# Performance work log

Measured on AMD Instinct MI355X. Metric: run time of the kernel, lower is better.

Reference implementation:

```python
import jax, jax.numpy as jnp
import numpy as np

ALPHA = 0.2  # LeakyReLU negative slope
MASK_FILL = -9e15


def setup_inputs() -> dict:
    key = jax.random.key(0)
    k1, k2, k3, k4 = jax.random.split(key, 4)
    N, F_IN, F_OUT = 8192, 128, 64
    x = jax.random.normal(k1, (N, F_IN), dtype=jnp.float32)
    adj = jax.random.randint(k2, (N, N), 0, 2, dtype=jnp.int32)
    # xavier_uniform with gain=1.414 (approx sqrt(2))
    gain = 1.414
    lim_w = gain * np.sqrt(6.0 / (F_IN + F_OUT))
    W = jax.random.uniform(k3, (F_IN, F_OUT), minval=-lim_w, maxval=lim_w, dtype=jnp.float32)
    lim_a = gain * np.sqrt(6.0 / (2 * F_OUT + 1))
    a = jax.random.uniform(k4, (2 * F_OUT, 1), minval=-lim_a, maxval=lim_a, dtype=jnp.float32)
    return {"x": x, "adj": adj, "W": W, "a": a}


def reference(x, adj, W, a):
    # h: [N, F_out]
    h = x @ W
    f_out = h.shape[1]
    # Decompose a^T [h_i || h_j] = h_i . a1 + h_j . a2 (exactly the same math,
    # avoids materializing the N*N*2F concat tensor).
    a1 = a[:f_out, 0]  # [F_out]
    a2 = a[f_out:, 0]  # [F_out]
    e = (h @ a1)[:, None] + (h @ a2)[None, :]  # [N, N]
    e = jax.nn.leaky_relu(e, negative_slope=ALPHA)
    e = jnp.where(adj > 0, e, MASK_FILL)
    attention = jax.nn.softmax(e, axis=1)  # row-wise softmax
    h_prime = attention @ h  # [N, F_out]
    return jax.nn.elu(h_prime)  # concat=True branch
```

## Files before the change

kernel.cpp:

```cpp
#include <hip/hip_runtime.h>
#include <math.h>

#define NN 8192
#define FIN 128
#define FOUT 64
#define LRELU 0.2f
#define JSPLIT 8
#define BI 64
#define PASTR 72
#define HTSTR 72

typedef _Float16 f16x8 __attribute__((ext_vector_type(8)));
typedef _Float16 f16x4 __attribute__((ext_vector_type(4)));
typedef float f32x4 __attribute__((ext_vector_type(4)));

#define WS_HT 0
#define WS_S1 262144
#define WS_S2 270336
#define WS_S2MAX 278528
#define WS_PACC 278544
#define WS_LP (WS_PACC + JSPLIT * NN * FOUT)

__global__ __launch_bounds__(256) void k_hs(const float* __restrict__ x,
                                            const float* __restrict__ W,
                                            const float* __restrict__ a,
                                            float* ws) {
  __shared__ float Wl[FIN * FOUT];
  __shared__ float xl[16 * FIN];
  __shared__ float hl[16 * FOUT];
  const int t = threadIdx.x;
  const int i0 = blockIdx.x * 16;

#pragma unroll
  for (int c = 0; c < 8; ++c) {
    const int flat = c * 1024 + t * 4;
    *(float4*)&Wl[flat] = *(const float4*)&W[flat];
  }
#pragma unroll
  for (int c = 0; c < 2; ++c) {
    const int flat = c * 1024 + t * 4;
    *(float4*)&xl[flat] = *(const float4*)&x[(size_t)i0 * FIN + flat];
  }
  __syncthreads();

  const int r = t >> 4;
  const int fg = t & 15;
  float4 acc = make_float4(0.f, 0.f, 0.f, 0.f);
#pragma unroll 4
  for (int k = 0; k < FIN; ++k) {
    const float xv = xl[r * FIN + k];
    const float4 wv = *(const float4*)&Wl[k * FOUT + fg * 4];
    acc.x = fmaf(xv, wv.x, acc.x);
    acc.y = fmaf(xv, wv.y, acc.y);
    acc.z = fmaf(xv, wv.z, acc.z);
    acc.w = fmaf(xv, wv.w, acc.w);
  }

  float v1 = acc.x * a[fg * 4] + acc.y * a[fg * 4 + 1] +
             acc.z * a[fg * 4 + 2] + acc.w * a[fg * 4 + 3];
  float v2 = acc.x * a[FOUT + fg * 4] + acc.y * a[FOUT + fg * 4 + 1] +
             acc.z * a[FOUT + fg * 4 + 2] + acc.w * a[FOUT + fg * 4 + 3];
  v1 += __shfl_xor(v1, 1); v2 += __shfl_xor(v2, 1);
  v1 += __shfl_xor(v1, 2); v2 += __shfl_xor(v2, 2);
  v1 += __shfl_xor(v1, 4); v2 += __shfl_xor(v2, 4);
  v1 += __shfl_xor(v1, 8); v2 += __shfl_xor(v2, 8);
  if (fg == 0) {
    ws[WS_S1 + i0 + r] = v1;
    ws[WS_S2 + i0 + r] = v2;
  }

  *(float4*)&hl[r * FOUT + fg * 4] = acc;
  __syncthreads();
  _Float16* ht = (_Float16*)(ws + WS_HT);
  if (t < 128) {
    const int f = t >> 1;
    const int off = (t & 1) * 8;
    f16x8 tmp;
#pragma unroll
    for (int u = 0; u < 8; ++u) tmp[u] = (_Float16)hl[(off + u) * FOUT + f];
    *(f16x8*)&ht[(size_t)f * NN + i0 + off] = tmp;
  }
}

__global__ __launch_bounds__(256) void k_s2max(float* ws) {
  __shared__ float red[256];
  const int t = threadIdx.x;
  float v = -1e30f;
#pragma unroll
  for (int i = 0; i < NN / 256; ++i) v = fmaxf(v, ws[WS_S2 + i * 256 + t]);
  red[t] = v;
  __syncthreads();
  for (int s = 128; s >= 1; s >>= 1) {
    if (t < s) red[t] = fmaxf(red[t], red[t + s]);
    __syncthreads();
  }
  if (t == 0) ws[WS_S2MAX] = red[0];
}

__global__ __launch_bounds__(256) void k_main(const int* __restrict__ adj,
                                              float* ws) {
  __shared__ __align__(16) _Float16 pal[BI * PASTR];
  __shared__ __align__(16) _Float16 htl[FOUT * HTSTR];
  __shared__ float s1l[BI], mll[BI];

  const int t = threadIdx.x;
  const int ib = blockIdx.x >> 3;
  const int js = blockIdx.x & 7;
  const int i0 = ib * BI;
  const int jbase = js * (NN / JSPLIT);

  const _Float16* ht = (const _Float16*)(ws + WS_HT);
  const float s2max = ws[WS_S2MAX];
  if (t < BI) {
    const float s1v = ws[WS_S1 + i0 + t];
    s1l[t] = s1v;
    const float tmp = s1v + s2max;
    mll[t] = fmaxf(tmp, LRELU * tmp);
  }

  f32x4 acc[4];
#pragma unroll
  for (int nf = 0; nf < 4; ++nf) acc[nf] = (f32x4){0.f, 0.f, 0.f, 0.f};
  float lacc[4] = {0.f, 0.f, 0.f, 0.f};

  const int jg = t & 15;
  const int ig = t >> 4;
  const int w = t >> 6;
  const int l = t & 63;

  __syncthreads();

  for (int tile = 0; tile < (NN / JSPLIT) / 64; ++tile) {
    const int j0 = jbase + tile * 64;

#pragma unroll
    for (int c2 = 0; c2 < 2; ++c2) {
      const int chunk = t + c2 * 256;
      const int n = chunk >> 3, off = (chunk & 7) * 8;
      *(f16x8*)&htl[n * HTSTR + off] = *(const f16x8*)&ht[(size_t)n * NN + j0 + off];
    }

    const float4 s2v = *(const float4*)&ws[WS_S2 + j0 + jg * 4];
#pragma unroll
    for (int c = 0; c < 4; ++c) {
      const int il = ig + c * 16;
      const int4 av = *(const int4*)&adj[(size_t)(i0 + il) * NN + j0 + jg * 4];
      const float s1v = s1l[il], mv = mll[il];
      float e0 = s1v + s2v.x; e0 = fmaxf(e0, LRELU * e0);
      float e1 = s1v + s2v.y; e1 = fmaxf(e1, LRELU * e1);
      float e2 = s1v + s2v.z; e2 = fmaxf(e2, LRELU * e2);
      float e3 = s1v + s2v.w; e3 = fmaxf(e3, LRELU * e3);
      const _Float16 p0 = av.x > 0 ? (_Float16)__expf(e0 - mv) : (_Float16)0.f;
      const _Float16 p1 = av.y > 0 ? (_Float16)__expf(e1 - mv) : (_Float16)0.f;
      const _Float16 p2 = av.z > 0 ? (_Float16)__expf(e2 - mv) : (_Float16)0.f;
      const _Float16 p3 = av.w > 0 ? (_Float16)__expf(e3 - mv) : (_Float16)0.f;
      lacc[c] += ((float)p0 + (float)p1) + ((float)p2 + (float)p3);
      f16x4 pv = {p0, p1, p2, p3};
      *(f16x4*)&pal[il * PASTR + jg * 4] = pv;
    }
    __syncthreads();

    {
      const int mrow = w * 16 + (l & 15);
      const int q8 = (l >> 4) * 8;
      const f16x8 a0 = *(const f16x8*)&pal[mrow * PASTR + q8];
      const f16x8 a1 = *(const f16x8*)&pal[mrow * PASTR + 32 + q8];
#pragma unroll
      for (int nf = 0; nf < 4; ++nf) {
        const int nrow = nf * 16 + (l & 15);
        const f16x8 b0 = *(const f16x8*)&htl[nrow * HTSTR + q8];
        const f16x8 b1 = *(const f16x8*)&htl[nrow * HTSTR + 32 + q8];
        acc[nf] = __builtin_amdgcn_mfma_f32_16x16x32_f16(a0, b0, acc[nf], 0, 0, 0);
        acc[nf] = __builtin_amdgcn_mfma_f32_16x16x32_f16(a1, b1, acc[nf], 0, 0, 0);
      }
    }
    __syncthreads();
  }

#pragma unroll
  for (int c = 0; c < 4; ++c) {
    float v = lacc[c];
    v += __shfl_xor(v, 1);
    v += __shfl_xor(v, 2);
    v += __shfl_xor(v, 4);
    v += __shfl_xor(v, 8);
    if (jg == 0) ws[WS_LP + js * NN + i0 + ig + c * 16] = v;
  }

  float* pacc = ws + WS_PACC + (size_t)js * (NN * FOUT);
  const int orow = i0 + w * 16 + (l >> 4) * 4;
  const int ocol = l & 15;
#pragma unroll
  for (int nf = 0; nf < 4; ++nf)
#pragma unroll
    for (int r = 0; r < 4; ++r)
      pacc[(size_t)(orow + r) * FOUT + nf * 16 + ocol] = acc[nf][r];
}

__global__ __launch_bounds__(256) void k_combine(const float* __restrict__ ws,
                                                 float* __restrict__ out) {
  const int idx = blockIdx.x * 256 + threadIdx.x;
  const int i = idx >> 6;
  float s = 0.f, l = 0.f;
#pragma unroll
  for (int js = 0; js < JSPLIT; ++js) {
    s += ws[WS_PACC + (size_t)js * (NN * FOUT) + idx];
    l += ws[WS_LP + js * NN + i];
  }
  const float v = s / l;
  out[idx] = v > 0.f ? v : expm1f(v);
}

extern "C" void kernel_launch(void* const* d_in, const int* in_sizes, int n_in,
                              void* d_out, int out_size, void* d_ws,
                              size_t ws_size, hipStream_t stream) {
  const float* x = (const float*)d_in[0];
  const int* adj = (const int*)d_in[1];
  const float* W = (const float*)d_in[2];
  const float* a = (const float*)d_in[3];
  float* ws = (float*)d_ws;
  float* out = (float*)d_out;

  hipLaunchKernelGGL(k_hs, dim3(NN / 16), dim3(256), 0, stream, x, W, a, ws);
  hipLaunchKernelGGL(k_s2max, dim3(1), dim3(256), 0, stream, ws);
  hipLaunchKernelGGL(k_main, dim3((NN / BI) * JSPLIT), dim3(256), 0, stream,
                     adj, ws);
  hipLaunchKernelGGL(k_combine, dim3(NN * FOUT / 256), dim3(256), 0, stream,
                     ws, out);
}
```

Before: 414.1 us.

## Build MFMA A-fragments in registers from adj and stage whole h-chunk once

k_main now loads the block's entire 512-column slice of transposed h and s2 into LDS once, instead of reloading h per 64-column tile. Each lane computes its own softmax numerators straight from adj into the f16 MFMA A operand, so the P tile no longer goes through LDS and the two barriers per tile disappear. The exponent uses exp2f with a prescaled max. The launch also changes: 512-thread blocks of 128 rows, a j-split of 16, and launch_bounds(512,1). The cost is double the partial accumulator workspace and combine traffic, plus single-block occupancy because of the roughly 68 KB LDS footprint.

```diff
diff --git a/kernel.cpp b/kernel.cpp
--- a/kernel.cpp
+++ b/kernel.cpp
@@ -5,13 +5,12 @@
 #define FIN 128
 #define FOUT 64
 #define LRELU 0.2f
-#define JSPLIT 8
-#define BI 64
-#define PASTR 72
-#define HTSTR 72
+#define JSPLIT 16
+#define JCH (NN / JSPLIT)
+#define HTSTR 520
+#define L2E 1.44269504f
 
 typedef _Float16 f16x8 __attribute__((ext_vector_type(8)));
-typedef _Float16 f16x4 __attribute__((ext_vector_type(4)));
 typedef float f32x4 __attribute__((ext_vector_type(4)));
 
 #define WS_HT 0
@@ -97,99 +96,87 @@
   if (t == 0) ws[WS_S2MAX] = red[0];
 }
 
-__global__ __launch_bounds__(256) void k_main(const int* __restrict__ adj,
-                                              float* ws) {
-  __shared__ __align__(16) _Float16 pal[BI * PASTR];
+__global__ __launch_bounds__(512, 1) void k_main(const int* __restrict__ adj,
+                                                 float* ws) {
   __shared__ __align__(16) _Float16 htl[FOUT * HTSTR];
-  __shared__ float s1l[BI], mll[BI];
+  __shared__ float s2l[JCH];
 
   const int t = threadIdx.x;
-  const int ib = blockIdx.x >> 3;
-  const int js = blockIdx.x & 7;
-  const int i0 = ib * BI;
-  const int jbase = js * (NN / JSPLIT);
+  const int ib = blockIdx.x >> 4;
+  const int js = blockIdx.x & 15;
+  const int i0 = ib * 128;
+  const int jc0 = js * JCH;
 
   const _Float16* ht = (const _Float16*)(ws + WS_HT);
-  const float s2max = ws[WS_S2MAX];
-  if (t < BI) {
-    const float s1v = ws[WS_S1 + i0 + t];
-    s1l[t] = s1v;
-    const float tmp = s1v + s2max;
-    mll[t] = fmaxf(tmp, LRELU * tmp);
-  }
-
-  f32x4 acc[4];
-#pragma unroll
-  for (int nf = 0; nf < 4; ++nf) acc[nf] = (f32x4){0.f, 0.f, 0.f, 0.f};
-  float lacc[4] = {0.f, 0.f, 0.f, 0.f};
-
-  const int jg = t & 15;
-  const int ig = t >> 4;
+
+#pragma unroll
+  for (int c = 0; c < 8; ++c) {
+    const int chunk = c * 512 + t;
+    const int f = chunk >> 6;
+    const int off = (chunk & 63) * 8;
+    *(f16x8*)&htl[f * HTSTR + off] = *(const f16x8*)&ht[(size_t)f * NN + jc0 + off];
+  }
+  s2l[t] = ws[WS_S2 + jc0 + t];
+
   const int w = t >> 6;
   const int l = t & 63;
-
-  __syncthreads();
-
-  for (int tile = 0; tile < (NN / JSPLIT) / 64; ++tile) {
-    const int j0 = jbase + tile * 64;
-
-#pragma unroll
-    for (int c2 = 0; c2 < 2; ++c2) {
-      const int chunk = t + c2 * 256;
-      const int n = chunk >> 3, off = (chunk & 7) * 8;
-      *(f16x8*)&htl[n * HTSTR + off] = *(const f16x8*)&ht[(size_t)n * NN + j0 + off];
+  const int m16 = l & 15;
+  const int q8 = (l >> 4) * 8;
+  const int row = i0 + w * 16 + m16;
+
+  const float s2max = ws[WS_S2MAX];
+  const float s1v = ws[WS_S1 + row];
+  const float tmp0 = s1v + s2max;
+  const float mv = fmaxf(tmp0, LRELU * tmp0);
+  const float mneg = -mv * L2E;
+
+  f32x4 acc[4];
+#pragma unroll
+  for (int nf = 0; nf < 4; ++nf) acc[nf] = (f32x4){0.f, 0.f, 0.f, 0.f};
+  float lacc = 0.f;
+
+  const int* arow = adj + (size_t)row * NN + jc0 + q8;
+
+  __syncthreads();
+
+#pragma unroll 2
+  for (int it = 0; it < JCH / 32; ++it) {
+    const int4 a0 = *(const int4*)(arow + it * 32);
+    const int4 a1 = *(const int4*)(arow + it * 32 + 4);
+    const float4 s20 = *(const float4*)&s2l[it * 32 + q8];
+    const float4 s21 = *(const float4*)&s2l[it * 32 + q8 + 4];
+
+    float e, p[8];
+    e = s1v + s20.x; e = fmaxf(e, LRELU * e); p[0] = a0.x ? exp2f(fmaf(e, L2E, mneg)) : 0.f;
+    e = s1v + s20.y; e = fmaxf(e, LRELU * e); p[1] = a0.y ? exp2f(fmaf(e, L2E, mneg)) : 0.f;
+    e = s1v + s20.z; e = fmaxf(e, LRELU * e); p[2] = a0.z ? exp2f(fmaf(e, L2E, mneg)) : 0.f;
+    e = s1v + s20.w; e = fmaxf(e, LRELU * e); p[3] = a0.w ? exp2f(fmaf(e, L2E, mneg)) : 0.f;
+    e = s1v + s21.x; e = fmaxf(e, LRELU * e); p[4] = a1.x ? exp2f(fmaf(e, L2E, mneg)) : 0.f;
+    e = s1v + s21.y; e = fmaxf(e, LRELU * e); p[5] = a1.y ? exp2f(fmaf(e, L2E, mneg)) : 0.f;
+    e = s1v + s21.z; e = fmaxf(e, LRELU * e); p[6] = a1.z ? exp2f(fmaf(e, L2E, mneg)) : 0.f;
+    e = s1v + s21.w; e = fmaxf(e, LRELU * e); p[7] = a1.w ? exp2f(fmaf(e, L2E, mneg)) : 0.f;
+
+    f16x8 af;
+#pragma unroll
+    for (int u = 0; u < 8; ++u) af[u] = (_Float16)p[u];
+#pragma unroll
+    for (int u = 0; u < 8; ++u) lacc += (float)af[u];
+
+    const int kb = it * 32 + q8;
+#pragma unroll
+    for (int nf = 0; nf < 4; ++nf) {
+      const f16x8 b = *(const f16x8*)&htl[(nf * 16 + m16) * HTSTR + kb];
+      acc[nf] = __builtin_amdgcn_mfma_f32_16x16x32_f16(af, b, acc[nf], 0, 0, 0);
     }
-
-    const float4 s2v = *(const float4*)&ws[WS_S2 + j0 + jg * 4];
-#pragma unroll
-    for (int c = 0; c < 4; ++c) {
-      const int il = ig + c * 16;
-      const int4 av = *(const int4*)&adj[(size_t)(i0 + il) * NN + j0 + jg * 4];
-      const float s1v = s1l[il], mv = mll[il];
-      float e0 = s1v + s2v.x; e0 = fmaxf(e0, LRELU * e0);
-      float e1 = s1v + s2v.y; e1 = fmaxf(e1, LRELU * e1);
-      float e2 = s1v + s2v.z; e2 = fmaxf(e2, LRELU * e2);
-      float e3 = s1v + s2v.w; e3 = fmaxf(e3, LRELU * e3);
-      const _Float16 p0 = av.x > 0 ? (_Float16)__expf(e0 - mv) : (_Float16)0.f;
-      const _Float16 p1 = av.y > 0 ? (_Float16)__expf(e1 - mv) : (_Float16)0.f;
-      const _Float16 p2 = av.z > 0 ? (_Float16)__expf(e2 - mv) : (_Float16)0.f;
-      const _Float16 p3 = av.w > 0 ? (_Float16)__expf(e3 - mv) : (_Float16)0.f;
-      lacc[c] += ((float)p0 + (float)p1) + ((float)p2 + (float)p3);
-      f16x4 pv = {p0, p1, p2, p3};
-      *(f16x4*)&pal[il * PASTR + jg * 4] = pv;
-    }
-    __syncthreads();
-
-    {
-      const int mrow = w * 16 + (l & 15);
-      const int q8 = (l >> 4) * 8;
-      const f16x8 a0 = *(const f16x8*)&pal[mrow * PASTR + q8];
-      const f16x8 a1 = *(const f16x8*)&pal[mrow * PASTR + 32 + q8];
-#pragma unroll
-      for (int nf = 0; nf < 4; ++nf) {
-        const int nrow = nf * 16 + (l & 15);
-        const f16x8 b0 = *(const f16x8*)&htl[nrow * HTSTR + q8];
-        const f16x8 b1 = *(const f16x8*)&htl[nrow * HTSTR + 32 + q8];
-        acc[nf] = __builtin_amdgcn_mfma_f32_16x16x32_f16(a0, b0, acc[nf], 0, 0, 0);
-        acc[nf] = __builtin_amdgcn_mfma_f32_16x16x32_f16(a1, b1, acc[nf], 0, 0, 0);
-      }
-    }
-    __syncthreads();
-  }
-
-#pragma unroll
-  for (int c = 0; c < 4; ++c) {
-    float v = lacc[c];
-    v += __shfl_xor(v, 1);
-    v += __shfl_xor(v, 2);
-    v += __shfl_xor(v, 4);
-    v += __shfl_xor(v, 8);
-    if (jg == 0) ws[WS_LP + js * NN + i0 + ig + c * 16] = v;
-  }
+  }
+
+  lacc += __shfl_xor(lacc, 16);
+  lacc += __shfl_xor(lacc, 32);
+  if (l < 16) ws[WS_LP + js * NN + row] = lacc;
 
   float* pacc = ws + WS_PACC + (size_t)js * (NN * FOUT);
   const int orow = i0 + w * 16 + (l >> 4) * 4;
-  const int ocol = l & 15;
+  const int ocol = m16;
 #pragma unroll
   for (int nf = 0; nf < 4; ++nf)
 #pragma unroll
@@ -223,7 +210,7 @@
 
   hipLaunchKernelGGL(k_hs, dim3(NN / 16), dim3(256), 0, stream, x, W, a, ws);
   hipLaunchKernelGGL(k_s2max, dim3(1), dim3(256), 0, stream, ws);
-  hipLaunchKernelGGL(k_main, dim3((NN / BI) * JSPLIT), dim3(256), 0, stream,
+  hipLaunchKernelGGL(k_main, dim3((NN / 128) * JSPLIT), dim3(512), 0, stream,
                      adj, ws);
   hipLaunchKernelGGL(k_combine, dim3(NN * FOUT / 256), dim3(256), 0, stream,
                      ws, out);
```

Measured after the change: 391.1 us. -5.6%, faster.
